# Kernel tuning notes

Hardware: AMD Instinct MI355X
Metric: run time of the kernel (lower is better)

The kernel has to match this reference:

```python
import jax, jax.numpy as jnp
import numpy as np

N_NODES = 20000   # max_childs
N_EDGES = 640000
FEAT = 256        # node_feat_size
HID = 128         # node_hidden_size
NUM_SEM = 57
EDGE_TYPES = 4
EDGE_FEAT = 8


def setup_inputs() -> dict:
    key = jax.random.key(0)
    ks = jax.random.split(key, 10)
    inp = {
        "child_feats": jax.random.normal(ks[0], (1, N_NODES, FEAT + NUM_SEM), jnp.float32),
        "child_exists": jnp.ones((1, N_NODES, 1), jnp.float32),
        "edge_type_onehot": jax.random.uniform(ks[1], (1, N_EDGES, EDGE_TYPES), jnp.float32),
        "edge_feats": jax.random.normal(ks[2], (1, N_EDGES, EDGE_FEAT), jnp.float32),
        "edge_indices": jax.random.randint(ks[3], (1, N_EDGES, 2), 0, N_NODES, jnp.int64 if jax.config.jax_enable_x64 else jnp.int32),
        "W_child": jax.random.normal(ks[4], (FEAT + NUM_SEM, HID), jnp.float32) * 0.05,
        "b_child": jnp.zeros((HID,), jnp.float32),
        "W_edge0": jax.random.normal(ks[5], (2 * HID + EDGE_FEAT + EDGE_TYPES, HID), jnp.float32) * 0.05,
        "b_edge0": jnp.zeros((HID,), jnp.float32),
        "W_edge1": jax.random.normal(ks[6], (2 * HID + EDGE_FEAT + EDGE_TYPES, HID), jnp.float32) * 0.05,
        "b_edge1": jnp.zeros((HID,), jnp.float32),
        "W_parent": jax.random.normal(ks[7], (3 * HID, FEAT), jnp.float32) * 0.05,
        "b_parent": jnp.zeros((FEAT,), jnp.float32),
    }
    return inp


def reference(child_feats, child_exists, edge_type_onehot, edge_feats, edge_indices,
              W_child, b_child, W_edge0, b_edge0, W_edge1, b_edge1, W_parent, b_parent):
    # child_op + existence mask: [1, N, FEAT+NUM_SEM] -> [N, HID]
    h = jax.nn.relu(child_feats @ W_child + b_child) * child_exists
    h = h[0]  # batch_size is hard-coded to 1 in the original module

    # symmetric_type == 'max': pool over children
    iter_parent_feats = [jnp.max(h, axis=0)]

    # edge features: cat(edge_type_onehot, edge_feats) -> [E, ET+EF]
    ef = jnp.concatenate([edge_type_onehot[0], edge_feats[0]], axis=1)
    src = edge_indices[0, :, 0]
    dst = edge_indices[0, :, 1]

    for W, b in ((W_edge0, b_edge0), (W_edge1, b_edge1)):
        # gather -> per-edge MLP: [E, 2*HID + ET + EF] -> [E, HID]
        msg = jax.nn.relu(jnp.concatenate([h[src], h[dst], ef], axis=1) @ W + b)
        # edge_symmetric_type == 'max' with zero-initialized out buffer:
        # result = max(0, segment_max(msg)) per node
        h = jnp.maximum(jax.ops.segment_max(msg, src, num_segments=N_NODES), 0.0)
        iter_parent_feats.append(jnp.max(h, axis=0))

    parent = jnp.concatenate(iter_parent_feats)[None, :]  # [1, 3*HID]
    return jax.nn.relu(parent @ W_parent + b_parent)       # [1, FEAT]
```

## Files before the change

kernel.cpp:

```cpp
#include <hip/hip_runtime.h>

#define N_NODES   20000
#define N_EDGES   640000
#define CF        313
#define KC        320
#define ROWB      640

typedef __attribute__((ext_vector_type(8))) short short8;
typedef __attribute__((ext_vector_type(4))) float f32x4;
typedef __attribute__((ext_vector_type(4))) unsigned short u16x4;
typedef float f32x4u __attribute__((ext_vector_type(4), aligned(4)));
typedef _Float16 h2 __attribute__((ext_vector_type(2)));

static __device__ __forceinline__ unsigned short f2bf(float f) {
    unsigned u = __float_as_uint(f);
    u = u + 0x7FFFu + ((u >> 16) & 1u);
    return (unsigned short)(u >> 16);
}
static __device__ __forceinline__ int pkh(float a, float b) {
    h2 h; h.x = (_Float16)a; h.y = (_Float16)b;
    return __builtin_bit_cast(int, h);
}
static __device__ __forceinline__ h2 bch(int v) { return __builtin_bit_cast(h2, v); }
static __device__ __forceinline__ float dot2f(h2 a, h2 b, float c) {
    return __builtin_amdgcn_fdot2(a, b, c, false);
}

__global__ void setup_kernel(const float* __restrict__ Wc,
                             const float* __restrict__ We0,
                             const float* __restrict__ We1,
                             const int* __restrict__ eidx,
                             unsigned short* __restrict__ WcT,
                             unsigned short* __restrict__ Wab0,
                             unsigned short* __restrict__ Wab1,
                             unsigned* __restrict__ hist) {
    const int b = blockIdx.x, tid = threadIdx.x;
    if (b < 416) {
        int g = b * 256 + tid;
        if (g < 128 * KC) {
            int n = g / KC, k = g % KC;
            WcT[g] = f2bf(k < CF ? Wc[k * 128 + n] : 0.f);
        } else if (g < 128 * KC + 32768) {
            int h = g - 128 * KC;
            int n = h >> 7, k = h & 127;
            Wab0[h] = f2bf(n < 128 ? We0[k * 128 + n] : We0[(128 + k) * 128 + (n - 128)]);
        } else {
            int h = g - 128 * KC - 32768;
            int n = h >> 7, k = h & 127;
            Wab1[h] = f2bf(n < 128 ? We1[k * 128 + n] : We1[(128 + k) * 128 + (n - 128)]);
        }
    } else {
        int e = (b - 416) * 256 + tid;
        if (e < N_EDGES) atomicAdd(hist + eidx[2 * e], 1u);
    }
}

__global__ void scan_kernel(const unsigned* __restrict__ hist,
                            unsigned* __restrict__ cursor,
                            unsigned* __restrict__ cstart,
                            unsigned* __restrict__ parent) {
    __shared__ unsigned part[1024];
    int t = threadIdx.x;
    if (t < 384) parent[t] = 0;
    unsigned loc[20];
    unsigned s = 0;
    int base = t * 20;
    if (t < 1000) {
        #pragma unroll
        for (int i = 0; i < 20; ++i) { loc[i] = hist[base + i]; s += loc[i]; }
    }
    part[t] = s;
    __syncthreads();
    for (int off = 1; off < 1024; off <<= 1) {
        unsigned u = (t >= off) ? part[t - off] : 0u;
        __syncthreads();
        part[t] += u;
        __syncthreads();
    }
    if (t < 1000) {
        unsigned run = part[t] - s;
        #pragma unroll
        for (int i = 0; i < 20; ++i) {
            cursor[base + i] = run;
            cstart[base + i] = run;
            run += loc[i];
        }
    }
}

__global__ void scatter_kernel(const int* __restrict__ eidx,
                               const float* __restrict__ onehot,
                               const float* __restrict__ efeat,
                               unsigned* __restrict__ cursor,
                               int4* __restrict__ es) {
    int e = blockIdx.x * 256 + threadIdx.x;
    if (e >= N_EDGES) return;
    int2 sd = ((const int2*)eidx)[e];
    unsigned pos = atomicAdd(cursor + sd.x, 1u);
    float4 oh = *(const float4*)(onehot + 4 * (size_t)e);
    float4 ea = *(const float4*)(efeat + 8 * (size_t)e);
    float4 eb = *(const float4*)(efeat + 8 * (size_t)e + 4);
    int4 w0, w1;
    w0.x = sd.y;
    w0.y = pkh(oh.x, oh.y); w0.z = pkh(oh.z, oh.w); w0.w = pkh(ea.x, ea.y);
    w1.x = pkh(ea.z, ea.w); w1.y = pkh(eb.x, eb.y); w1.z = pkh(eb.z, eb.w);
    w1.w = 0;
    es[2 * (size_t)pos]     = w0;
    es[2 * (size_t)pos + 1] = w1;
}

__global__ __launch_bounds__(256)
void child_ab(const float* __restrict__ cf,
              const float* __restrict__ exists,
              const unsigned short* __restrict__ WcT,
              const float* __restrict__ bc,
              const unsigned short* __restrict__ Wab,
              const float* __restrict__ be,
              float* __restrict__ Afl,
              unsigned short* __restrict__ Bbf,
              unsigned int* __restrict__ pmax) {
    __shared__ __align__(16) unsigned char Alds[64 * ROWB];
    __shared__ __align__(16) unsigned char Hlds[64 * 256];

    const int tid  = threadIdx.x;
    const int lane = tid & 63;
    const int wave = tid >> 6;
    const int row0 = blockIdx.x * 64;

    const int n0c = wave * 32;
    short8 bfrag[10][2];
    {
        int col  = n0c + (lane & 15);
        int krow = (lane >> 4) * 8;
        #pragma unroll
        for (int ks = 0; ks < 10; ++ks)
            #pragma unroll
            for (int nt = 0; nt < 2; ++nt)
                bfrag[ks][nt] = *(const short8*)(WcT + (col + nt * 16) * KC + ks * 32 + krow);
    }
    float bvc[2];
    bvc[0] = bc[n0c + (lane & 15)];
    bvc[1] = bc[n0c + 16 + (lane & 15)];

    {
        int r = tid >> 2, p = tid & 3;
        int node = row0 + r;
        bool valid = node < N_NODES;
        const float* g = cf + (size_t)node * CF;
        unsigned rbase = r * ROWB;
        unsigned sw = (r & 7) << 4;
        #pragma unroll
        for (int i = 0; i < 10; ++i) {
            int c = p + i * 4;
            short8 v = {};
            if (valid) {
                if (c < 39) {
                    f32x4u a0 = *(const f32x4u*)(g + c * 8);
                    f32x4u a1 = *(const f32x4u*)(g + c * 8 + 4);
                    v[0] = (short)f2bf(a0.x); v[1] = (short)f2bf(a0.y);
                    v[2] = (short)f2bf(a0.z); v[3] = (short)f2bf(a0.w);
                    v[4] = (short)f2bf(a1.x); v[5] = (short)f2bf(a1.y);
                    v[6] = (short)f2bf(a1.z); v[7] = (short)f2bf(a1.w);
                } else {
                    v[0] = (short)f2bf(g[312]);
                }
            }
            *(short8*)(Alds + ((rbase + c * 16) ^ sw)) = v;
        }
    }
    __syncthreads();

    f32x4 acc[4][2] = {};
    {
        int arow = lane & 15;
        unsigned kb = (lane >> 4) * 16;
        #pragma unroll
        for (int ks = 0; ks < 10; ++ks)
            #pragma unroll
            for (int mt = 0; mt < 4; ++mt) {
                int row = mt * 16 + arow;
                short8 a = *(const short8*)(Alds + (((unsigned)row * ROWB + ks * 64 + kb) ^ ((row & 7) << 4)));
                acc[mt][0] = __builtin_amdgcn_mfma_f32_16x16x32_bf16(a, bfrag[ks][0], acc[mt][0], 0, 0, 0);
                acc[mt][1] = __builtin_amdgcn_mfma_f32_16x16x32_bf16(a, bfrag[ks][1], acc[mt][1], 0, 0, 0);
            }
    }

    {
        int rb = (lane >> 4) * 4;
        #pragma unroll
        for (int nt = 0; nt < 2; ++nt) {
            int col = n0c + nt * 16 + (lane & 15);
            float m = 0.f;
            #pragma unroll
            for (int mt = 0; mt < 4; ++mt)
                #pragma unroll
                for (int j = 0; j < 4; ++j) {
                    int r = mt * 16 + rb + j;
                    int node = row0 + r;
                    float v = 0.f;
                    if (node < N_NODES)
                        v = fmaxf(acc[mt][nt][j] + bvc[nt], 0.f) * exists[node];
                    *(unsigned short*)(Hlds + (((unsigned)r * 256 + col * 2) ^ ((r & 7) << 4))) = f2bf(v);
                    m = fmaxf(m, v);
                }
            m = fmaxf(m, __shfl_xor(m, 16));
            m = fmaxf(m, __shfl_xor(m, 32));
            if ((lane >> 4) == 0)
                atomicMax(pmax + col, __float_as_uint(m));
        }
    }
    __syncthreads();

    const int n0 = wave * 64;
    const int krow = (lane >> 4) * 8;
    short8 bfrag2[4][4];
    {
        int colb = n0 + (lane & 15);
        #pragma unroll
        for (int ks = 0; ks < 4; ++ks)
            #pragma unroll
            for (int nt = 0; nt < 4; ++nt)
                bfrag2[ks][nt] = *(const short8*)(Wab + (colb + nt * 16) * 128 + ks * 32 + krow);
    }

    f32x4 acc2[4][4] = {};
    #pragma unroll
    for (int ks = 0; ks < 4; ++ks)
        #pragma unroll
        for (int mt = 0; mt < 4; ++mt) {
            int r = mt * 16 + (lane & 15);
            short8 a = *(const short8*)(Hlds + (((unsigned)r * 256 + ks * 64 + krow * 2) ^ ((r & 7) << 4)));
            #pragma unroll
            for (int nt = 0; nt < 4; ++nt)
                acc2[mt][nt] = __builtin_amdgcn_mfma_f32_16x16x32_bf16(a, bfrag2[ks][nt], acc2[mt][nt], 0, 0, 0);
        }

    {
        int rb = (lane >> 4) * 4;
        #pragma unroll
        for (int nt = 0; nt < 4; ++nt) {
            int col = n0 + nt * 16 + (lane & 15);
            float badd = (col < 128) ? be[col] : 0.f;
            #pragma unroll
            for (int mt = 0; mt < 4; ++mt)
                #pragma unroll
                for (int j = 0; j < 4; ++j) {
                    int row = row0 + mt * 16 + rb + j;
                    if (row < N_NODES) {
                        float v = acc2[mt][nt][j] + badd;
                        if (col < 128) Afl[(size_t)row * 128 + col] = v;
                        else           Bbf[(size_t)row * 128 + col - 128] = f2bf(v);
                    }
                }
        }
    }
}

__global__ __launch_bounds__(256)
void gemmAB(const unsigned short* __restrict__ hbf,
            const unsigned short* __restrict__ WT,
            const float* __restrict__ bias,
            float* __restrict__ Afl,
            unsigned short* __restrict__ Bbf) {
    const int tid  = threadIdx.x;
    const int lane = tid & 63;
    const int wave = tid >> 6;
    const int n0   = wave * 64;
    const int row0 = blockIdx.x * 64;
    const int krow = (lane >> 4) * 8;

    short8 bfrag[4][4];
    {
        int colb = n0 + (lane & 15);
        #pragma unroll
        for (int ks = 0; ks < 4; ++ks)
            #pragma unroll
            for (int nt = 0; nt < 4; ++nt)
                bfrag[ks][nt] = *(const short8*)(WT + (colb + nt * 16) * 128 + ks * 32 + krow);
    }

    f32x4 acc[4][4] = {};
    #pragma unroll
    for (int ks = 0; ks < 4; ++ks)
        #pragma unroll
        for (int mt = 0; mt < 4; ++mt) {
            int row = row0 + mt * 16 + (lane & 15);
            row = min(row, N_NODES - 1);
            short8 a = *(const short8*)(hbf + (size_t)row * 128 + ks * 32 + krow);
            #pragma unroll
            for (int nt = 0; nt < 4; ++nt)
                acc[mt][nt] = __builtin_amdgcn_mfma_f32_16x16x32_bf16(a, bfrag[ks][nt], acc[mt][nt], 0, 0, 0);
        }

    {
        int rb = (lane >> 4) * 4;
        #pragma unroll
        for (int nt = 0; nt < 4; ++nt) {
            int col = n0 + nt * 16 + (lane & 15);
            float badd = (col < 128) ? bias[col] : 0.f;
            #pragma unroll
            for (int mt = 0; mt < 4; ++mt)
                #pragma unroll
                for (int j = 0; j < 4; ++j) {
                    int row = row0 + mt * 16 + rb + j;
                    if (row < N_NODES) {
                        float v = acc[mt][nt][j] + badd;
                        if (col < 128) Afl[(size_t)row * 128 + col] = v;
                        else           Bbf[(size_t)row * 128 + col - 128] = f2bf(v);
                    }
                }
        }
    }
}

__global__ __launch_bounds__(256, 3)
void edge_pass(const unsigned short* __restrict__ Bbf,
               const float* __restrict__ Afl,
               const int4* __restrict__ es,
               const float* __restrict__ Wef,
               const unsigned* __restrict__ cstart,
               const unsigned* __restrict__ hist,
               unsigned short* __restrict__ hbf,
               unsigned* __restrict__ pslice) {
    __shared__ unsigned cmax[128];
    const int tid = threadIdx.x;
    if (tid < 128) cmax[tid] = 0;
    __syncthreads();

    const int s  = blockIdx.x * 8 + (tid >> 5);
    const int c0 = (tid & 31) * 4;

    float4 a = *(const float4*)(Afl + (size_t)s * 128 + c0);

    h2 wf[6][4];
    #pragma unroll
    for (int kp = 0; kp < 6; ++kp)
        #pragma unroll
        for (int j = 0; j < 4; ++j) {
            h2 w;
            w.x = (_Float16)Wef[(2 * kp) * 128 + c0 + j];
            w.y = (_Float16)Wef[(2 * kp + 1) * 128 + c0 + j];
            wf[kp][j] = w;
        }

    float m0 = -1e30f, m1 = -1e30f, m2 = -1e30f, m3 = -1e30f;
    const unsigned cnt = hist[s];
    if (cnt) {
        const unsigned last = cnt - 1;
        const unsigned cb = cstart[s] * 32u;
        const char* esb = (const char*)es;
        const unsigned short* bbase = Bbf + c0;

        unsigned dstv[12];
        int4 ra[3], rb[3];
        u16x4 bv[6];

        #pragma unroll
        for (int k = 0; k < 12; ++k)
            dstv[k] = *(const unsigned*)(esb + cb + min((unsigned)k, last) * 32u);
        #pragma unroll
        for (int k = 0; k < 3; ++k) {
            const int4* q = (const int4*)(esb + cb + min((unsigned)k, last) * 32u);
            ra[k] = q[0]; rb[k] = q[1];
        }
        #pragma unroll
        for (int k = 0; k < 6; ++k)
            bv[k] = *(const u16x4*)(bbase + (size_t)dstv[k] * 128);

        const unsigned niter = (cnt + 11) / 12;
        for (unsigned it = 0; it < niter; ++it) {
            const unsigned jb = it * 12;
            #pragma unroll
            for (int u = 0; u < 12; ++u) {
                int4 RA = ra[u % 3], RB = rb[u % 3];
                u16x4 B = bv[u % 6];
                h2 e0 = bch(RA.y), e1 = bch(RA.z), e2 = bch(RA.w);
                h2 e3 = bch(RB.x), e4 = bch(RB.y), e5 = bch(RB.z);

                float x0 = __uint_as_float(((unsigned)(unsigned short)B[0]) << 16);
                float x1 = __uint_as_float(((unsigned)(unsigned short)B[1]) << 16);
                float x2 = __uint_as_float(((unsigned)(unsigned short)B[2]) << 16);
                float x3 = __uint_as_float(((unsigned)(unsigned short)B[3]) << 16);
                x0 = dot2f(e0, wf[0][0], x0); x1 = dot2f(e0, wf[0][1], x1);
                x2 = dot2f(e0, wf[0][2], x2); x3 = dot2f(e0, wf[0][3], x3);
                x0 = dot2f(e1, wf[1][0], x0); x1 = dot2f(e1, wf[1][1], x1);
                x2 = dot2f(e1, wf[1][2], x2); x3 = dot2f(e1, wf[1][3], x3);
                x0 = dot2f(e2, wf[2][0], x0); x1 = dot2f(e2, wf[2][1], x1);
                x2 = dot2f(e2, wf[2][2], x2); x3 = dot2f(e2, wf[2][3], x3);
                x0 = dot2f(e3, wf[3][0], x0); x1 = dot2f(e3, wf[3][1], x1);
                x2 = dot2f(e3, wf[3][2], x2); x3 = dot2f(e3, wf[3][3], x3);
                x0 = dot2f(e4, wf[4][0], x0); x1 = dot2f(e4, wf[4][1], x1);
                x2 = dot2f(e4, wf[4][2], x2); x3 = dot2f(e4, wf[4][3], x3);
                x0 = dot2f(e5, wf[5][0], x0); x1 = dot2f(e5, wf[5][1], x1);
                x2 = dot2f(e5, wf[5][2], x2); x3 = dot2f(e5, wf[5][3], x3);
                m0 = fmaxf(m0, x0); m1 = fmaxf(m1, x1);
                m2 = fmaxf(m2, x2); m3 = fmaxf(m3, x3);

                unsigned jd = min(jb + u + 12u, last);
                dstv[u] = *(const unsigned*)(esb + cb + jd * 32u);
                unsigned jr = min(jb + u + 3u, last);
                const int4* q = (const int4*)(esb + cb + jr * 32u);
                ra[u % 3] = q[0]; rb[u % 3] = q[1];
                bv[u % 6] = *(const u16x4*)(bbase + (size_t)dstv[(u + 6) % 12] * 128);
            }
        }
    }

    float h0 = fmaxf(a.x + m0, 0.f), h1 = fmaxf(a.y + m1, 0.f);
    float h2v = fmaxf(a.z + m2, 0.f), h3 = fmaxf(a.w + m3, 0.f);

    unsigned lo = (unsigned)f2bf(h0) | ((unsigned)f2bf(h1) << 16);
    unsigned hi = (unsigned)f2bf(h2v) | ((unsigned)f2bf(h3) << 16);
    *(uint2*)(hbf + (size_t)s * 128 + c0) = make_uint2(lo, hi);

    float g0 = fmaxf(h0, __shfl_xor(h0, 32));
    float g1 = fmaxf(h1, __shfl_xor(h1, 32));
    float g2 = fmaxf(h2v, __shfl_xor(h2v, 32));
    float g3 = fmaxf(h3, __shfl_xor(h3, 32));
    if ((tid & 63) < 32) {
        atomicMax(&cmax[c0],     __float_as_uint(g0));
        atomicMax(&cmax[c0 + 1], __float_as_uint(g1));
        atomicMax(&cmax[c0 + 2], __float_as_uint(g2));
        atomicMax(&cmax[c0 + 3], __float_as_uint(g3));
    }
    __syncthreads();
    if (tid < 128) atomicMax(pslice + tid, cmax[tid]);
}

__global__ void final_gemm(const float* __restrict__ parent,
                           const float* __restrict__ Wp,
                           const float* __restrict__ bp,
                           float* __restrict__ out) {
    __shared__ float p[384];
    __shared__ float red[256];
    int t = threadIdx.x;
    for (int i = t; i < 384; i += 256) p[i] = parent[i];
    __syncthreads();
    int col = blockIdx.x * 16 + (t & 15);
    int kc  = t >> 4;
    float s = 0.f;
    for (int k = kc * 24; k < kc * 24 + 24; ++k) s += p[k] * Wp[k * 256 + col];
    red[t] = s;
    __syncthreads();
    #pragma unroll
    for (int off = 8; off >= 1; off >>= 1) {
        if (kc < off) red[t] += red[t + off * 16];
        __syncthreads();
    }
    if (t < 16) out[col] = fmaxf(red[t] + bp[col], 0.f);
}

extern "C" void kernel_launch(void* const* d_in, const int* in_sizes, int n_in,
                              void* d_out, int out_size, void* d_ws, size_t ws_size,
                              hipStream_t stream) {
    const float* child_feats  = (const float*)d_in[0];
    const float* child_exists = (const float*)d_in[1];
    const float* onehot       = (const float*)d_in[2];
    const float* efeat        = (const float*)d_in[3];
    const int*   eidx         = (const int*)d_in[4];
    const float* Wc  = (const float*)d_in[5];
    const float* bc  = (const float*)d_in[6];
    const float* We0 = (const float*)d_in[7];
    const float* be0 = (const float*)d_in[8];
    const float* We1 = (const float*)d_in[9];
    const float* be1 = (const float*)d_in[10];
    const float* Wp  = (const float*)d_in[11];
    const float* bp  = (const float*)d_in[12];

    char* ws = (char*)d_ws;
    unsigned short* hbf    = (unsigned short*)(ws);
    float*          Afl    = (float*)(ws + 5120000);
    unsigned short* Bbf    = (unsigned short*)(ws + 15360000);
    int4*           es     = (int4*)(ws + 20480000);
    unsigned short* WcT    = (unsigned short*)(ws + 40960000);
    unsigned short* Wab0   = (unsigned short*)(ws + 41041920);
    unsigned short* Wab1   = (unsigned short*)(ws + 41107456);
    unsigned*       parent = (unsigned*)(ws + 41172992);
    unsigned*       hist   = (unsigned*)(ws + 41174528);
    unsigned*       cstart = (unsigned*)(ws + 41254528);
    unsigned*       cursor = (unsigned*)(ws + 41334592);

    const float* Wef0 = We0 + 256 * 128;
    const float* Wef1 = We1 + 256 * 128;

    hipMemsetAsync(hist, 0, N_NODES * 4, stream);

    setup_kernel<<<2916, 256, 0, stream>>>(Wc, We0, We1, eidx, WcT, Wab0, Wab1, hist);
    scan_kernel<<<1, 1024, 0, stream>>>(hist, cursor, cstart, parent);
    scatter_kernel<<<2500, 256, 0, stream>>>(eidx, onehot, efeat, cursor, es);

    child_ab<<<313, 256, 0, stream>>>(child_feats, child_exists, WcT, bc,
                                      Wab0, be0, Afl, Bbf, parent);

    edge_pass<<<2500, 256, 0, stream>>>(Bbf, Afl, es, Wef0, cstart, hist, hbf, parent + 128);

    gemmAB<<<313, 256, 0, stream>>>(hbf, Wab1, be1, Afl, Bbf);
    edge_pass<<<2500, 256, 0, stream>>>(Bbf, Afl, es, Wef1, cstart, hist, hbf, parent + 256);

    final_gemm<<<16, 256, 0, stream>>>((const float*)parent, Wp, bp, (float*)d_out);
}
```

Before: 268.3 us.

## Split each node's edge list across two half-waves in edge pass

Each source node is now handled by a full 64-lane wave, with each 32-lane half processing half of the node's edges. The two partial maxima are combined with a cross-half shuffle, and the grid doubles to 5000 blocks. This doubles the number of independent gather streams in flight, which shortens the serial per-node loop and adds memory-level parallelism. In exchange, each wave does less work per launch, the per-wave weight loading is duplicated, and short edge lists incur more tail overhead.

```diff
diff --git a/kernel.cpp b/kernel.cpp
--- a/kernel.cpp
+++ b/kernel.cpp
@@ -327,10 +327,11 @@
     if (tid < 128) cmax[tid] = 0;
     __syncthreads();
 
-    const int s  = blockIdx.x * 8 + (tid >> 5);
-    const int c0 = (tid & 31) * 4;
-
-    float4 a = *(const float4*)(Afl + (size_t)s * 128 + c0);
+    const int s    = blockIdx.x * 4 + (tid >> 6);
+    const int half = (tid >> 5) & 1;
+    const int c0   = (tid & 31) * 4;
+
+    f32x4 a = *(const f32x4*)(Afl + (size_t)s * 128 + c0);
 
     h2 wf[6][4];
     #pragma unroll
@@ -344,10 +345,13 @@
         }
 
     float m0 = -1e30f, m1 = -1e30f, m2 = -1e30f, m3 = -1e30f;
-    const unsigned cnt = hist[s];
-    if (cnt) {
-        const unsigned last = cnt - 1;
-        const unsigned cb = cstart[s] * 32u;
+    const unsigned cntf  = hist[s];
+    const unsigned h0c   = cntf >> 1;
+    const unsigned mycnt = half ? (cntf - h0c) : h0c;
+    const unsigned ebase = cstart[s] + (half ? h0c : 0u);
+    if (mycnt) {
+        const unsigned last = mycnt - 1;
+        const unsigned cb = ebase * 32u;
         const char* esb = (const char*)es;
         const unsigned short* bbase = Bbf + c0;
 
@@ -367,7 +371,7 @@
         for (int k = 0; k < 6; ++k)
             bv[k] = *(const u16x4*)(bbase + (size_t)dstv[k] * 128);
 
-        const unsigned niter = (cnt + 11) / 12;
+        const unsigned niter = (mycnt + 11) / 12;
         for (unsigned it = 0; it < niter; ++it) {
             const unsigned jb = it * 12;
             #pragma unroll
@@ -406,22 +410,23 @@
         }
     }
 
-    float h0 = fmaxf(a.x + m0, 0.f), h1 = fmaxf(a.y + m1, 0.f);
-    float h2v = fmaxf(a.z + m2, 0.f), h3 = fmaxf(a.w + m3, 0.f);
-
-    unsigned lo = (unsigned)f2bf(h0) | ((unsigned)f2bf(h1) << 16);
-    unsigned hi = (unsigned)f2bf(h2v) | ((unsigned)f2bf(h3) << 16);
-    *(uint2*)(hbf + (size_t)s * 128 + c0) = make_uint2(lo, hi);
-
-    float g0 = fmaxf(h0, __shfl_xor(h0, 32));
-    float g1 = fmaxf(h1, __shfl_xor(h1, 32));
-    float g2 = fmaxf(h2v, __shfl_xor(h2v, 32));
-    float g3 = fmaxf(h3, __shfl_xor(h3, 32));
-    if ((tid & 63) < 32) {
-        atomicMax(&cmax[c0],     __float_as_uint(g0));
-        atomicMax(&cmax[c0 + 1], __float_as_uint(g1));
-        atomicMax(&cmax[c0 + 2], __float_as_uint(g2));
-        atomicMax(&cmax[c0 + 3], __float_as_uint(g3));
+    m0 = fmaxf(m0, __shfl_xor(m0, 32));
+    m1 = fmaxf(m1, __shfl_xor(m1, 32));
+    m2 = fmaxf(m2, __shfl_xor(m2, 32));
+    m3 = fmaxf(m3, __shfl_xor(m3, 32));
+
+    if (half == 0) {
+        float h0 = fmaxf(a.x + m0, 0.f), h1 = fmaxf(a.y + m1, 0.f);
+        float h2v = fmaxf(a.z + m2, 0.f), h3 = fmaxf(a.w + m3, 0.f);
+
+        unsigned lo = (unsigned)f2bf(h0) | ((unsigned)f2bf(h1) << 16);
+        unsigned hi = (unsigned)f2bf(h2v) | ((unsigned)f2bf(h3) << 16);
+        *(uint2*)(hbf + (size_t)s * 128 + c0) = make_uint2(lo, hi);
+
+        atomicMax(&cmax[c0],     __float_as_uint(h0));
+        atomicMax(&cmax[c0 + 1], __float_as_uint(h1));
+        atomicMax(&cmax[c0 + 2], __float_as_uint(h2v));
+        atomicMax(&cmax[c0 + 3], __float_as_uint(h3));
     }
     __syncthreads();
     if (tid < 128) atomicMax(pslice + tid, cmax[tid]);
@@ -492,10 +497,10 @@
     child_ab<<<313, 256, 0, stream>>>(child_feats, child_exists, WcT, bc,
                                       Wab0, be0, Afl, Bbf, parent);
 
-    edge_pass<<<2500, 256, 0, stream>>>(Bbf, Afl, es, Wef0, cstart, hist, hbf, parent + 128);
+    edge_pass<<<5000, 256, 0, stream>>>(Bbf, Afl, es, Wef0, cstart, hist, hbf, parent + 128);
 
     gemmAB<<<313, 256, 0, stream>>>(hbf, Wab1, be1, Afl, Bbf);
-    edge_pass<<<2500, 256, 0, stream>>>(Bbf, Afl, es, Wef1, cstart, hist, hbf, parent + 256);
+    edge_pass<<<5000, 256, 0, stream>>>(Bbf, Afl, es, Wef1, cstart, hist, hbf, parent + 256);
 
     final_gemm<<<16, 256, 0, stream>>>((const float*)parent, Wp, bp, (float*)d_out);
 }
```

After: 365.5 us. +36.2%, slower.

## Use atomic work queue for dynamic node scheduling in edge passes

Applied to the files above, without the earlier changes.

Edge passes move from one node per half-wave over a fixed grid to a persistent-style loop. Each half-wave takes its next node index from a global atomic counter, which the scan kernel resets. This is meant to balance the uneven per-node edge counts and to amortize the weight-register setup across nodes, at the cost of one atomic per node and a shuffle. The launch-bounds occupancy hint is also dropped, and gemmAB is retiled to 32 rows per block with twice as many blocks and no bounds guards, since the node count divides evenly.

```diff
diff --git a/kernel.cpp b/kernel.cpp
--- a/kernel.cpp
+++ b/kernel.cpp
@@ -58,10 +58,12 @@
 __global__ void scan_kernel(const unsigned* __restrict__ hist,
                             unsigned* __restrict__ cursor,
                             unsigned* __restrict__ cstart,
-                            unsigned* __restrict__ parent) {
+                            unsigned* __restrict__ parent,
+                            unsigned* __restrict__ qctr) {
     __shared__ unsigned part[1024];
     int t = threadIdx.x;
     if (t < 384) parent[t] = 0;
+    if (t == 0) { qctr[0] = 0; qctr[1] = 0; }
     unsigned loc[20];
     unsigned s = 0;
     int base = t * 20;
@@ -266,7 +268,7 @@
     const int lane = tid & 63;
     const int wave = tid >> 6;
     const int n0   = wave * 64;
-    const int row0 = blockIdx.x * 64;
+    const int row0 = blockIdx.x * 32;
     const int krow = (lane >> 4) * 8;
 
     short8 bfrag[4][4];
@@ -279,13 +281,12 @@
                 bfrag[ks][nt] = *(const short8*)(WT + (colb + nt * 16) * 128 + ks * 32 + krow);
     }
 
-    f32x4 acc[4][4] = {};
+    f32x4 acc[2][4] = {};
     #pragma unroll
     for (int ks = 0; ks < 4; ++ks)
         #pragma unroll
-        for (int mt = 0; mt < 4; ++mt) {
+        for (int mt = 0; mt < 2; ++mt) {
             int row = row0 + mt * 16 + (lane & 15);
-            row = min(row, N_NODES - 1);
             short8 a = *(const short8*)(hbf + (size_t)row * 128 + ks * 32 + krow);
             #pragma unroll
             for (int nt = 0; nt < 4; ++nt)
@@ -299,27 +300,26 @@
             int col = n0 + nt * 16 + (lane & 15);
             float badd = (col < 128) ? bias[col] : 0.f;
             #pragma unroll
-            for (int mt = 0; mt < 4; ++mt)
+            for (int mt = 0; mt < 2; ++mt)
                 #pragma unroll
                 for (int j = 0; j < 4; ++j) {
                     int row = row0 + mt * 16 + rb + j;
-                    if (row < N_NODES) {
-                        float v = acc[mt][nt][j] + badd;
-                        if (col < 128) Afl[(size_t)row * 128 + col] = v;
-                        else           Bbf[(size_t)row * 128 + col - 128] = f2bf(v);
-                    }
+                    float v = acc[mt][nt][j] + badd;
+                    if (col < 128) Afl[(size_t)row * 128 + col] = v;
+                    else           Bbf[(size_t)row * 128 + col - 128] = f2bf(v);
                 }
         }
     }
 }
 
-__global__ __launch_bounds__(256, 3)
+__global__ __launch_bounds__(256)
 void edge_pass(const unsigned short* __restrict__ Bbf,
                const float* __restrict__ Afl,
                const int4* __restrict__ es,
                const float* __restrict__ Wef,
                const unsigned* __restrict__ cstart,
                const unsigned* __restrict__ hist,
+               unsigned* __restrict__ qctr,
                unsigned short* __restrict__ hbf,
                unsigned* __restrict__ pslice) {
     __shared__ unsigned cmax[128];
@@ -327,10 +327,7 @@
     if (tid < 128) cmax[tid] = 0;
     __syncthreads();
 
-    const int s  = blockIdx.x * 8 + (tid >> 5);
     const int c0 = (tid & 31) * 4;
-
-    float4 a = *(const float4*)(Afl + (size_t)s * 128 + c0);
 
     h2 wf[6][4];
     #pragma unroll
@@ -343,85 +340,87 @@
             wf[kp][j] = w;
         }
 
-    float m0 = -1e30f, m1 = -1e30f, m2 = -1e30f, m3 = -1e30f;
-    const unsigned cnt = hist[s];
-    if (cnt) {
-        const unsigned last = cnt - 1;
-        const unsigned cb = cstart[s] * 32u;
-        const char* esb = (const char*)es;
-        const unsigned short* bbase = Bbf + c0;
-
-        unsigned dstv[12];
-        int4 ra[3], rb[3];
-        u16x4 bv[6];
-
-        #pragma unroll
-        for (int k = 0; k < 12; ++k)
-            dstv[k] = *(const unsigned*)(esb + cb + min((unsigned)k, last) * 32u);
-        #pragma unroll
-        for (int k = 0; k < 3; ++k) {
-            const int4* q = (const int4*)(esb + cb + min((unsigned)k, last) * 32u);
-            ra[k] = q[0]; rb[k] = q[1];
-        }
-        #pragma unroll
-        for (int k = 0; k < 6; ++k)
-            bv[k] = *(const u16x4*)(bbase + (size_t)dstv[k] * 128);
-
-        const unsigned niter = (cnt + 11) / 12;
-        for (unsigned it = 0; it < niter; ++it) {
-            const unsigned jb = it * 12;
-            #pragma unroll
-            for (int u = 0; u < 12; ++u) {
-                int4 RA = ra[u % 3], RB = rb[u % 3];
-                u16x4 B = bv[u % 6];
-                h2 e0 = bch(RA.y), e1 = bch(RA.z), e2 = bch(RA.w);
-                h2 e3 = bch(RB.x), e4 = bch(RB.y), e5 = bch(RB.z);
-
-                float x0 = __uint_as_float(((unsigned)(unsigned short)B[0]) << 16);
-                float x1 = __uint_as_float(((unsigned)(unsigned short)B[1]) << 16);
-                float x2 = __uint_as_float(((unsigned)(unsigned short)B[2]) << 16);
-                float x3 = __uint_as_float(((unsigned)(unsigned short)B[3]) << 16);
-                x0 = dot2f(e0, wf[0][0], x0); x1 = dot2f(e0, wf[0][1], x1);
-                x2 = dot2f(e0, wf[0][2], x2); x3 = dot2f(e0, wf[0][3], x3);
-                x0 = dot2f(e1, wf[1][0], x0); x1 = dot2f(e1, wf[1][1], x1);
-                x2 = dot2f(e1, wf[1][2], x2); x3 = dot2f(e1, wf[1][3], x3);
-                x0 = dot2f(e2, wf[2][0], x0); x1 = dot2f(e2, wf[2][1], x1);
-                x2 = dot2f(e2, wf[2][2], x2); x3 = dot2f(e2, wf[2][3], x3);
-                x0 = dot2f(e3, wf[3][0], x0); x1 = dot2f(e3, wf[3][1], x1);
-                x2 = dot2f(e3, wf[3][2], x2); x3 = dot2f(e3, wf[3][3], x3);
-                x0 = dot2f(e4, wf[4][0], x0); x1 = dot2f(e4, wf[4][1], x1);
-                x2 = dot2f(e4, wf[4][2], x2); x3 = dot2f(e4, wf[4][3], x3);
-                x0 = dot2f(e5, wf[5][0], x0); x1 = dot2f(e5, wf[5][1], x1);
-                x2 = dot2f(e5, wf[5][2], x2); x3 = dot2f(e5, wf[5][3], x3);
-                m0 = fmaxf(m0, x0); m1 = fmaxf(m1, x1);
-                m2 = fmaxf(m2, x2); m3 = fmaxf(m3, x3);
-
-                unsigned jd = min(jb + u + 12u, last);
-                dstv[u] = *(const unsigned*)(esb + cb + jd * 32u);
-                unsigned jr = min(jb + u + 3u, last);
-                const int4* q = (const int4*)(esb + cb + jr * 32u);
-                ra[u % 3] = q[0]; rb[u % 3] = q[1];
-                bv[u % 6] = *(const u16x4*)(bbase + (size_t)dstv[(u + 6) % 12] * 128);
+    for (;;) {
+        unsigned s;
+        if ((tid & 31) == 0) s = atomicAdd(qctr, 1u);
+        s = (unsigned)__shfl((int)s, (int)(threadIdx.x & 32));
+        if (s >= N_NODES) break;
+
+        f32x4 a = *(const f32x4*)(Afl + (size_t)s * 128 + c0);
+        float m0 = -1e30f, m1 = -1e30f, m2 = -1e30f, m3 = -1e30f;
+        const unsigned cnt = hist[s];
+        if (cnt) {
+            const unsigned last = cnt - 1;
+            const unsigned cb = cstart[s] * 32u;
+            const char* esb = (const char*)es;
+            const unsigned short* bbase = Bbf + c0;
+
+            unsigned dstv[12];
+            int4 ra[3], rb[3];
+            u16x4 bv[6];
+
+            #pragma unroll
+            for (int k = 0; k < 12; ++k)
+                dstv[k] = *(const unsigned*)(esb + cb + min((unsigned)k, last) * 32u);
+            #pragma unroll
+            for (int k = 0; k < 3; ++k) {
+                const int4* q = (const int4*)(esb + cb + min((unsigned)k, last) * 32u);
+                ra[k] = q[0]; rb[k] = q[1];
             }
-        }
-    }
-
-    float h0 = fmaxf(a.x + m0, 0.f), h1 = fmaxf(a.y + m1, 0.f);
-    float h2v = fmaxf(a.z + m2, 0.f), h3 = fmaxf(a.w + m3, 0.f);
-
-    unsigned lo = (unsigned)f2bf(h0) | ((unsigned)f2bf(h1) << 16);
-    unsigned hi = (unsigned)f2bf(h2v) | ((unsigned)f2bf(h3) << 16);
-    *(uint2*)(hbf + (size_t)s * 128 + c0) = make_uint2(lo, hi);
-
-    float g0 = fmaxf(h0, __shfl_xor(h0, 32));
-    float g1 = fmaxf(h1, __shfl_xor(h1, 32));
-    float g2 = fmaxf(h2v, __shfl_xor(h2v, 32));
-    float g3 = fmaxf(h3, __shfl_xor(h3, 32));
-    if ((tid & 63) < 32) {
-        atomicMax(&cmax[c0],     __float_as_uint(g0));
-        atomicMax(&cmax[c0 + 1], __float_as_uint(g1));
-        atomicMax(&cmax[c0 + 2], __float_as_uint(g2));
-        atomicMax(&cmax[c0 + 3], __float_as_uint(g3));
+            #pragma unroll
+            for (int k = 0; k < 6; ++k)
+                bv[k] = *(const u16x4*)(bbase + (size_t)dstv[k] * 128);
+
+            const unsigned niter = (cnt + 11) / 12;
+            for (unsigned it = 0; it < niter; ++it) {
+                const unsigned jb = it * 12;
+                #pragma unroll
+                for (int u = 0; u < 12; ++u) {
+                    int4 RA = ra[u % 3], RB = rb[u % 3];
+                    u16x4 B = bv[u % 6];
+                    h2 e0 = bch(RA.y), e1 = bch(RA.z), e2 = bch(RA.w);
+                    h2 e3 = bch(RB.x), e4 = bch(RB.y), e5 = bch(RB.z);
+
+                    float x0 = __uint_as_float(((unsigned)(unsigned short)B[0]) << 16);
+                    float x1 = __uint_as_float(((unsigned)(unsigned short)B[1]) << 16);
+                    float x2 = __uint_as_float(((unsigned)(unsigned short)B[2]) << 16);
+                    float x3 = __uint_as_float(((unsigned)(unsigned short)B[3]) << 16);
+                    x0 = dot2f(e0, wf[0][0], x0); x1 = dot2f(e0, wf[0][1], x1);
+                    x2 = dot2f(e0, wf[0][2], x2); x3 = dot2f(e0, wf[0][3], x3);
+                    x0 = dot2f(e1, wf[1][0], x0); x1 = dot2f(e1, wf[1][1], x1);
+                    x2 = dot2f(e1, wf[1][2], x2); x3 = dot2f(e1, wf[1][3], x3);
+                    x0 = dot2f(e2, wf[2][0], x0); x1 = dot2f(e2, wf[2][1], x1);
+                    x2 = dot2f(e2, wf[2][2], x2); x3 = dot2f(e2, wf[2][3], x3);
+                    x0 = dot2f(e3, wf[3][0], x0); x1 = dot2f(e3, wf[3][1], x1);
+                    x2 = dot2f(e3, wf[3][2], x2); x3 = dot2f(e3, wf[3][3], x3);
+                    x0 = dot2f(e4, wf[4][0], x0); x1 = dot2f(e4, wf[4][1], x1);
+                    x2 = dot2f(e4, wf[4][2], x2); x3 = dot2f(e4, wf[4][3], x3);
+                    x0 = dot2f(e5, wf[5][0], x0); x1 = dot2f(e5, wf[5][1], x1);
+                    x2 = dot2f(e5, wf[5][2], x2); x3 = dot2f(e5, wf[5][3], x3);
+                    m0 = fmaxf(m0, x0); m1 = fmaxf(m1, x1);
+                    m2 = fmaxf(m2, x2); m3 = fmaxf(m3, x3);
+
+                    unsigned jd = min(jb + u + 12u, last);
+                    dstv[u] = *(const unsigned*)(esb + cb + jd * 32u);
+                    unsigned jr = min(jb + u + 3u, last);
+                    const int4* q = (const int4*)(esb + cb + jr * 32u);
+                    ra[u % 3] = q[0]; rb[u % 3] = q[1];
+                    bv[u % 6] = *(const u16x4*)(bbase + (size_t)dstv[(u + 6) % 12] * 128);
+                }
+            }
+        }
+
+        float h0 = fmaxf(a.x + m0, 0.f), h1 = fmaxf(a.y + m1, 0.f);
+        float h2v = fmaxf(a.z + m2, 0.f), h3 = fmaxf(a.w + m3, 0.f);
+
+        unsigned lo = (unsigned)f2bf(h0) | ((unsigned)f2bf(h1) << 16);
+        unsigned hi = (unsigned)f2bf(h2v) | ((unsigned)f2bf(h3) << 16);
+        *(uint2*)(hbf + (size_t)s * 128 + c0) = make_uint2(lo, hi);
+
+        atomicMax(&cmax[c0],     __float_as_uint(h0));
+        atomicMax(&cmax[c0 + 1], __float_as_uint(h1));
+        atomicMax(&cmax[c0 + 2], __float_as_uint(h2v));
+        atomicMax(&cmax[c0 + 3], __float_as_uint(h3));
     }
     __syncthreads();
     if (tid < 128) atomicMax(pslice + tid, cmax[tid]);
@@ -479,6 +478,7 @@
     unsigned*       hist   = (unsigned*)(ws + 41174528);
     unsigned*       cstart = (unsigned*)(ws + 41254528);
     unsigned*       cursor = (unsigned*)(ws + 41334592);
+    unsigned*       qctr   = (unsigned*)(ws + 41414592);
 
     const float* Wef0 = We0 + 256 * 128;
     const float* Wef1 = We1 + 256 * 128;
@@ -486,16 +486,18 @@
     hipMemsetAsync(hist, 0, N_NODES * 4, stream);
 
     setup_kernel<<<2916, 256, 0, stream>>>(Wc, We0, We1, eidx, WcT, Wab0, Wab1, hist);
-    scan_kernel<<<1, 1024, 0, stream>>>(hist, cursor, cstart, parent);
+    scan_kernel<<<1, 1024, 0, stream>>>(hist, cursor, cstart, parent, qctr);
     scatter_kernel<<<2500, 256, 0, stream>>>(eidx, onehot, efeat, cursor, es);
 
     child_ab<<<313, 256, 0, stream>>>(child_feats, child_exists, WcT, bc,
                                       Wab0, be0, Afl, Bbf, parent);
 
-    edge_pass<<<2500, 256, 0, stream>>>(Bbf, Afl, es, Wef0, cstart, hist, hbf, parent + 128);
-
-    gemmAB<<<313, 256, 0, stream>>>(hbf, Wab1, be1, Afl, Bbf);
-    edge_pass<<<2500, 256, 0, stream>>>(Bbf, Afl, es, Wef1, cstart, hist, hbf, parent + 256);
+    edge_pass<<<2048, 256, 0, stream>>>(Bbf, Afl, es, Wef0, cstart, hist,
+                                        qctr + 0, hbf, parent + 128);
+
+    gemmAB<<<625, 256, 0, stream>>>(hbf, Wab1, be1, Afl, Bbf);
+    edge_pass<<<2048, 256, 0, stream>>>(Bbf, Afl, es, Wef1, cstart, hist,
+                                        qctr + 1, hbf, parent + 256);
 
     final_gemm<<<16, 256, 0, stream>>>((const float*)parent, Wp, bp, (float*)d_out);
 }
```

Measured after the change: 568.2 us. 112% more time.
